# Optimization experiments

Measured on AMD Instinct MI355X. Metric: run time of the kernel, lower is better.

## Reference

```python
import jax, jax.numpy as jnp
import numpy as np

B, C, L = 8, 512, 2048


def setup_inputs() -> dict:
    key = jax.random.key(0)
    ks = jax.random.split(key, 7)
    s = 1.0 / np.sqrt(C)
    return {
        "x": jax.random.normal(ks[0], (B, C, L), dtype=jnp.float32),
        "Wq": jax.random.normal(ks[1], (C, C), dtype=jnp.float32) * s,
        "bq": jax.random.normal(ks[2], (C,), dtype=jnp.float32) * s,
        "Wk": jax.random.normal(ks[3], (C, C), dtype=jnp.float32) * s,
        "bk": jax.random.normal(ks[4], (C,), dtype=jnp.float32) * s,
        "Wv": jax.random.normal(ks[5], (C, C), dtype=jnp.float32) * s,
        "bv": jax.random.normal(ks[6], (C,), dtype=jnp.float32) * s,
    }


def reference(x, Wq, bq, Wk, bk, Wv, bv):
    # Conv1d(kernel_size=1) == per-position linear: [C_out, C_in] @ x[b,:,l]
    q = jnp.einsum('oi,bil->bol', Wq, x) + bq[None, :, None]  # [B, C, L]
    k = jnp.einsum('oi,bil->bol', Wk, x) + bk[None, :, None]
    v = jnp.einsum('oi,bil->bol', Wv, x) + bv[None, :, None]
    scale = 1.0 / jnp.sqrt(jnp.asarray(x.shape[1], dtype=x.dtype))
    # scores[b, l, m] = sum_c q[b,c,l] * k[b,c,m] / sqrt(C)
    scores = jnp.einsum('bcl,bcm->blm', q, k) * scale  # [B, L, L]
    attn = jax.nn.softmax(scores, axis=-1)
    # out[b, c, l] = sum_m v[b,c,m] * attn[b,l,m]   (== bmm(V, attn^T))
    return jnp.einsum('bcm,blm->bcl', v, attn)  # [B, C, L]
```

## Files before the change

### kernel.cpp

```cpp
#include <hip/hip_runtime.h>
#include <hip/hip_bf16.h>
#include <math.h>

#define B 8
#define C 512
#define L 2048

using bf16x8 = __bf16 __attribute__((ext_vector_type(8)));
using f32x4  = float __attribute__((ext_vector_type(4)));

#define MFMA(a, b, c) __builtin_amdgcn_mfma_f32_16x16x32_bf16((a), (b), (c), 0, 0, 0)
#define SC2 0.06375872f
#define SH2 -17.312340f

__device__ __forceinline__ unsigned short f2bf(float f) {
    unsigned int u; __builtin_memcpy(&u, &f, 4);
    u += 0x7FFF + ((u >> 16) & 1);
    return (unsigned short)(u >> 16);
}
__device__ __forceinline__ void load_lds16(const unsigned short* g, unsigned short* l) {
    __builtin_amdgcn_global_load_lds(
        (const __attribute__((address_space(1))) unsigned int*)g,
        (__attribute__((address_space(3))) unsigned int*)l, 16, 0, 0);
}

template<int MODE, int KDIM>
__device__ __forceinline__ void gemm_core(
    const unsigned short* __restrict__ A,
    const unsigned short* __restrict__ Bm,
    unsigned short* As, unsigned short* Bs,
    void* __restrict__ OutV, int ldo,
    float* __restrict__ ep)
{
    const int t = threadIdx.x;
    const int wave = t >> 6, lane = t & 63;
    const int ll = t & 15, quad = (t >> 4) & 3;
    const int lr = lane >> 2, chunk = lane & 3;
    const int wm = (wave & 1) * 64, wn = (wave >> 1) * 64;

    const unsigned short* gA0 = A  + (size_t)(wave * 32 + lr) * KDIM + chunk * 8;
    const unsigned short* gB0 = Bm + (size_t)(wave * 32 + lr) * KDIM + chunk * 8;
    unsigned short* lA0 = As + (wave * 32) * 32;
    unsigned short* lB0 = Bs + (wave * 32) * 32;
    const int P1 = 128 * 32;

    f32x4 acc[4][4];
#pragma unroll
    for (int i = 0; i < 4; ++i)
#pragma unroll
        for (int j = 0; j < 4; ++j) acc[i][j] = (f32x4){0.f, 0.f, 0.f, 0.f};

#pragma unroll 1
    for (int k0 = 0; k0 < KDIM; k0 += 64) {
        __syncthreads();
        load_lds16(gA0 + k0, lA0);
        load_lds16(gA0 + (size_t)16 * KDIM + k0, lA0 + 16 * 32);
        load_lds16(gA0 + k0 + 32, lA0 + P1);
        load_lds16(gA0 + (size_t)16 * KDIM + k0 + 32, lA0 + P1 + 16 * 32);
        load_lds16(gB0 + k0, lB0);
        load_lds16(gB0 + (size_t)16 * KDIM + k0, lB0 + 16 * 32);
        load_lds16(gB0 + k0 + 32, lB0 + P1);
        load_lds16(gB0 + (size_t)16 * KDIM + k0 + 32, lB0 + P1 + 16 * 32);
        __syncthreads();

#pragma unroll
        for (int p = 0; p < 2; ++p) {
            bf16x8 af[4], bf[4];
#pragma unroll
            for (int mi = 0; mi < 4; ++mi)
                af[mi] = *(const bf16x8*)&As[p * P1 + (wm + mi * 16 + ll) * 32 + quad * 8];
#pragma unroll
            for (int ni = 0; ni < 4; ++ni)
                bf[ni] = *(const bf16x8*)&Bs[p * P1 + (wn + ni * 16 + ll) * 32 + quad * 8];
#pragma unroll
            for (int mi = 0; mi < 4; ++mi)
#pragma unroll
                for (int ni = 0; ni < 4; ++ni)
                    acc[mi][ni] = MFMA(af[mi], bf[ni], acc[mi][ni]);
        }
    }

#pragma unroll
    for (int mi = 0; mi < 4; ++mi)
#pragma unroll
        for (int ni = 0; ni < 4; ++ni) {
            const int col = wn + ni * 16 + ll;
            float epc = 0.f;
            if (MODE == 0) epc = ep[col];
            if (MODE == 3) epc = 1.0f / ep[col];
#pragma unroll
            for (int r = 0; r < 4; ++r) {
                const int row = wm + mi * 16 + quad * 4 + r;
                float v = acc[mi][ni][r];
                if (MODE == 0)      v += epc;
                else if (MODE == 1) v += ep[row];
                else                v *= epc;
                if (MODE == 3)
                    ((float*)OutV)[(size_t)row * ldo + col] = v;
                else
                    ((unsigned short*)OutV)[(size_t)row * ldo + col] = f2bf(v);
            }
        }
}

__global__ __launch_bounds__(256) void prep(
    const float* __restrict__ x, const float* __restrict__ Wq,
    const float* __restrict__ Wk, const float* __restrict__ Wv,
    unsigned short* __restrict__ xt, unsigned short* __restrict__ o,
    float* __restrict__ rsum)
{
    __shared__ float tile[64][69];
    const int t = threadIdx.x;
    const int flat = blockIdx.x + 32 * (blockIdx.y + 8 * blockIdx.z);

    if (flat < 768) {
        if (flat < 16) {
            float4 z = make_float4(0.f, 0.f, 0.f, 0.f);
            *(float4*)(rsum + (flat * 256 + t) * 4) = z;
        }
        const int i = (flat * 256 + t) * 4;
        const int which = i >> 18;
        const int off = i & 0x3FFFF;
        const float* src = (which == 0) ? Wq : (which == 1) ? Wk : Wv;
        float4 v = *(const float4*)(src + off);
        union { unsigned short h[4]; uint2 u; } pk;
        pk.h[0] = f2bf(v.x); pk.h[1] = f2bf(v.y); pk.h[2] = f2bf(v.z); pk.h[3] = f2bf(v.w);
        *(uint2*)(o + i) = pk.u;
    }

    const int b = blockIdx.z, l0 = blockIdx.x * 64, c0 = blockIdx.y * 64;
    const int lx = t & 15, cy = t >> 4;
    const float* xb = x + (size_t)b * C * L;
#pragma unroll
    for (int p = 0; p < 4; ++p) {
        float4 v = *(const float4*)(xb + (size_t)(c0 + p * 16 + cy) * L + l0 + lx * 4);
        tile[p * 16 + cy][lx * 4 + 0] = v.x;
        tile[p * 16 + cy][lx * 4 + 1] = v.y;
        tile[p * 16 + cy][lx * 4 + 2] = v.z;
        tile[p * 16 + cy][lx * 4 + 3] = v.w;
    }
    __syncthreads();
    const int ocl = t & 15, ot = t >> 4;
    unsigned short* xtb = xt + (size_t)b * L * C;
#pragma unroll
    for (int p = 0; p < 4; ++p) {
        int ol = p * 16 + ot;
        union { unsigned short h[4]; uint2 u; } pk;
#pragma unroll
        for (int i = 0; i < 4; ++i) pk.h[i] = f2bf(tile[ocl * 4 + i][ol]);
        *(uint2*)(xtb + (size_t)(l0 + ol) * C + c0 + ocl * 4) = pk.u;
    }
}

__global__ __launch_bounds__(256) void qkv_gemm(
    const unsigned short* __restrict__ xt, const unsigned short* __restrict__ Wb,
    const float* __restrict__ bq, const float* __restrict__ bk,
    const float* __restrict__ bv,
    unsigned short* __restrict__ Qt, unsigned short* __restrict__ Kt,
    unsigned short* __restrict__ Vv)
{
    __shared__ unsigned short As[2 * 128 * 32], Bs[2 * 128 * 32];
    const int id = blockIdx.x;
    const int b = id & 7, r = id >> 3;
    const int which = r >> 6, tt = r & 63;
    const unsigned short* xtb = xt + (size_t)b * L * C;
    if (which < 2) {
        const int m0 = (tt & 15) * 128, n0 = (tt >> 4) * 128;
        const unsigned short* A  = xtb + (size_t)m0 * C;
        const unsigned short* Bm = Wb + (size_t)which * C * C + (size_t)n0 * C;
        unsigned short* Out = (which ? Kt : Qt) + (size_t)b * L * C
                              + (size_t)m0 * C + n0;
        gemm_core<0, C>(A, Bm, As, Bs, Out, C,
                        const_cast<float*>((which ? bk : bq) + n0));
    } else {
        const int m0 = (tt & 3) * 128, n0 = (tt >> 2) * 128;
        const unsigned short* A  = Wb + (size_t)2 * C * C + (size_t)m0 * C;
        const unsigned short* Bm = xtb + (size_t)n0 * C;
        unsigned short* Out = Vv + (size_t)b * C * L + (size_t)m0 * L + n0;
        gemm_core<1, C>(A, Bm, As, Bs, Out, L, const_cast<float*>(bv + m0));
    }
}

__global__ __launch_bounds__(512, 4) void sc_exp3(
    const unsigned short* __restrict__ Qt, const unsigned short* __restrict__ Kt,
    unsigned short* __restrict__ P, float* __restrict__ rsum,
    int hoff, int qrows, int mshift)
{
    __shared__ unsigned short As[256 * 64];
    __shared__ unsigned short Bs[128 * 64];
    constexpr int KD = C;

    const int id = blockIdx.x;
    const int b = id & 7, rr = id >> 3;
    const int m0 = (rr & ((1 << mshift) - 1)) * 256, n0 = (rr >> mshift) * 128;
    const unsigned short* A  = Qt + (size_t)b * L * C + (size_t)(hoff + m0) * C;
    const unsigned short* Bm = Kt + (size_t)b * L * C + (size_t)n0 * C;
    unsigned short* Out = P + (size_t)b * qrows * L + (size_t)m0 * L + n0;
    float* ep = rsum + (size_t)b * L + hoff + m0;

    const int t = threadIdx.x;
    const int wave = t >> 6, lane = t & 63;
    const int ll = t & 15, quad = (t >> 4) & 3;
    const int wm = (wave & 3) * 64, wn = (wave >> 2) * 64;

    const int r0 = t >> 3;
    const int swz = ((t & 7) ^ (r0 & 7)) * 8;
    const unsigned short* gA = A  + (size_t)r0 * KD + swz;
    const unsigned short* gB = Bm + (size_t)r0 * KD + swz;
    unsigned short* lA = As + wave * 512;
    unsigned short* lB = Bs + wave * 512;
    const int sw8 = ll & 7;

    f32x4 acc[4][4];
#pragma unroll
    for (int i = 0; i < 4; ++i)
#pragma unroll
        for (int j = 0; j < 4; ++j) acc[i][j] = (f32x4){0.f, 0.f, 0.f, 0.f};

#pragma unroll 1
    for (int k0 = 0; k0 < KD; k0 += 64) {
        __syncthreads();
        load_lds16(gA + k0,                     lA);
        load_lds16(gA + (size_t)64  * KD + k0,  lA + 64 * 64);
        load_lds16(gA + (size_t)128 * KD + k0,  lA + 128 * 64);
        load_lds16(gA + (size_t)192 * KD + k0,  lA + 192 * 64);
        load_lds16(gB + k0,                     lB);
        load_lds16(gB + (size_t)64  * KD + k0,  lB + 64 * 64);
        __syncthreads();

#pragma unroll
        for (int p = 0; p < 2; ++p) {
            bf16x8 af[4], bf[4];
#pragma unroll
            for (int mi = 0; mi < 4; ++mi)
                af[mi] = *(const bf16x8*)&As[(wm + mi * 16 + ll) * 64
                                             + ((p * 4 + quad) ^ sw8) * 8];
#pragma unroll
            for (int ni = 0; ni < 4; ++ni)
                bf[ni] = *(const bf16x8*)&Bs[(wn + ni * 16 + ll) * 64
                                             + ((p * 4 + quad) ^ sw8) * 8];
#pragma unroll
            for (int mi = 0; mi < 4; ++mi)
#pragma unroll
                for (int ni = 0; ni < 4; ++ni)
                    acc[mi][ni] = MFMA(af[mi], bf[ni], acc[mi][ni]);
        }
    }

    __syncthreads();
    unsigned* scratch = (unsigned*)As + wave * 1024;

    float rpart[4][4];
#pragma unroll
    for (int mi = 0; mi < 4; ++mi)
#pragma unroll
        for (int r = 0; r < 4; ++r) rpart[mi][r] = 0.f;

#pragma unroll
    for (int h = 0; h < 2; ++h) {
#pragma unroll
        for (int mi2 = 0; mi2 < 2; ++mi2) {
            const int mi = h * 2 + mi2;
#pragma unroll
            for (int ni = 0; ni < 4; ++ni)
#pragma unroll
                for (int r = 0; r < 4; ++r) {
                    float v = exp2f(fmaf(acc[mi][ni][r], SC2, SH2));
                    rpart[mi][r] += v;
                    unsigned bfv = f2bf(v);
                    unsigned pvv = (unsigned)__shfl_xor((int)bfv, 1, 64);
                    unsigned packed = (ll & 1) ? ((pvv & 0xFFFFu) | (bfv << 16))
                                               : ((bfv & 0xFFFFu) | (pvv << 16));
                    if (!(ll & 1))
                        scratch[(mi2 * 16 + quad * 4 + r) * 32 + ni * 8 + (ll >> 1)]
                            = packed;
                }
        }
#pragma unroll
        for (int i = 0; i < 4; ++i) {
            const int rl = i * 8 + (lane >> 3);
            uint4 d = *(const uint4*)(scratch + rl * 32 + (lane & 7) * 4);
            const int row = wm + h * 32 + rl;
            const int col = wn + (lane & 7) * 8;
            *(uint4*)&Out[(size_t)row * L + col] = d;
        }
    }

#pragma unroll
    for (int mi = 0; mi < 4; ++mi)
#pragma unroll
        for (int r = 0; r < 4; ++r) {
            float s = rpart[mi][r];
            s += __shfl_xor(s, 1, 64);
            s += __shfl_xor(s, 2, 64);
            s += __shfl_xor(s, 4, 64);
            s += __shfl_xor(s, 8, 64);
            if (ll == 0) atomicAdd(ep + wm + mi * 16 + quad * 4 + r, s);
        }
}

__global__ __launch_bounds__(256) void pv_gemm(
    const unsigned short* __restrict__ Vv, const unsigned short* __restrict__ P,
    const float* __restrict__ rsum, float* __restrict__ out,
    int hoff, int qrows)
{
    __shared__ unsigned short As[2 * 128 * 32], Bs[2 * 128 * 32];
    const int id = blockIdx.x;
    const int b = id & 7, r = id >> 3;
    const int m0 = (r & 3) * 128, n0 = (r >> 2) * 128;
    const unsigned short* A  = Vv + (size_t)b * C * L + (size_t)m0 * L;
    const unsigned short* Bm = P + (size_t)b * qrows * L + (size_t)n0 * L;
    float* Out = out + (size_t)b * C * L + (size_t)m0 * L + hoff + n0;
    float* ep = const_cast<float*>(rsum) + (size_t)b * L + hoff + n0;
    gemm_core<3, L>(A, Bm, As, Bs, Out, L, ep);
}

extern "C" void kernel_launch(void* const* d_in, const int* in_sizes, int n_in,
                              void* d_out, int out_size, void* d_ws, size_t ws_size,
                              hipStream_t stream) {
    const float* x  = (const float*)d_in[0];
    const float* Wq = (const float*)d_in[1];
    const float* bq = (const float*)d_in[2];
    const float* Wk = (const float*)d_in[3];
    const float* bk = (const float*)d_in[4];
    const float* Wv = (const float*)d_in[5];
    const float* bv = (const float*)d_in[6];
    float* out = (float*)d_out;

    const size_t BCL = (size_t)B * C * L;
    const bool fullP = ws_size >= 119078912ull;

    unsigned short* Qt = (unsigned short*)d_ws;
    unsigned short* Kt = Qt + BCL;
    unsigned short* Vv = Kt + BCL;
    unsigned short *Wb, *xt, *P;
    float* rsum;
    if (fullP) {
        Wb   = Vv + BCL;
        rsum = (float*)(Wb + (size_t)3 * C * C);
        xt   = (unsigned short*)(rsum + (size_t)B * L);
        P    = xt;
    } else {
        xt   = Vv + BCL;
        P    = xt;
        Wb   = P + (size_t)B * 1024 * L;
        rsum = (float*)(Wb + (size_t)3 * C * C);
    }

    prep<<<dim3(L / 64, C / 64, B), 256, 0, stream>>>(x, Wq, Wk, Wv, xt, Wb, rsum);
    qkv_gemm<<<dim3(1536), 256, 0, stream>>>(xt, Wb, bq, bk, bv, Qt, Kt, Vv);

    if (fullP) {
        sc_exp3<<<dim3(1024), 512, 0, stream>>>(Qt, Kt, P, rsum, 0, L, 3);
        pv_gemm<<<dim3(512), 256, 0, stream>>>(Vv, P, rsum, out, 0, L);
    } else {
        for (int h = 0; h < 2; ++h) {
            sc_exp3<<<dim3(512), 512, 0, stream>>>(Qt, Kt, P, rsum, h * 1024, 1024, 2);
            pv_gemm<<<dim3(256), 256, 0, stream>>>(Vv, P, rsum, out, h * 1024, 1024);
        }
    }
}
```

Baseline: 233.0 us.

## Add larger-tile PV GEMM kernel and write scores directly without LDS staging

Replaces the PV GEMM on the full-P path with a new 512-thread kernel. It uses 128x256 output tiles, a 64-deep K step and swizzled direct-to-LDS loads, and folds the 1/rowsum normalisation into its epilogue. The score/exp kernel also drops its LDS scratch repacking and the barrier before it, writing each bf16 probability straight to global memory. The larger tiles aim for more reuse per block. The direct scalar 2-byte stores remove a sync and LDS traffic but lose store coalescing and 16-byte vector writes. The new PV kernel has no double buffering and launches only 256 blocks, so it may leave compute units underused.

```diff
diff --git a/kernel.cpp b/kernel.cpp
--- a/kernel.cpp
+++ b/kernel.cpp
@@ -199,7 +199,7 @@
     float* ep = rsum + (size_t)b * L + hoff + m0;
 
     const int t = threadIdx.x;
-    const int wave = t >> 6, lane = t & 63;
+    const int wave = t >> 6;
     const int ll = t & 15, quad = (t >> 4) & 3;
     const int wm = (wave & 3) * 64, wn = (wave >> 2) * 64;
 
@@ -247,9 +247,6 @@
         }
     }
 
-    __syncthreads();
-    unsigned* scratch = (unsigned*)As + wave * 1024;
-
     float rpart[4][4];
 #pragma unroll
     for (int mi = 0; mi < 4; ++mi)
@@ -257,35 +254,18 @@
         for (int r = 0; r < 4; ++r) rpart[mi][r] = 0.f;
 
 #pragma unroll
-    for (int h = 0; h < 2; ++h) {
-#pragma unroll
-        for (int mi2 = 0; mi2 < 2; ++mi2) {
-            const int mi = h * 2 + mi2;
-#pragma unroll
-            for (int ni = 0; ni < 4; ++ni)
-#pragma unroll
-                for (int r = 0; r < 4; ++r) {
-                    float v = exp2f(fmaf(acc[mi][ni][r], SC2, SH2));
-                    rpart[mi][r] += v;
-                    unsigned bfv = f2bf(v);
-                    unsigned pvv = (unsigned)__shfl_xor((int)bfv, 1, 64);
-                    unsigned packed = (ll & 1) ? ((pvv & 0xFFFFu) | (bfv << 16))
-                                               : ((bfv & 0xFFFFu) | (pvv << 16));
-                    if (!(ll & 1))
-                        scratch[(mi2 * 16 + quad * 4 + r) * 32 + ni * 8 + (ll >> 1)]
-                            = packed;
-                }
-        }
-#pragma unroll
-        for (int i = 0; i < 4; ++i) {
-            const int rl = i * 8 + (lane >> 3);
-            uint4 d = *(const uint4*)(scratch + rl * 32 + (lane & 7) * 4);
-            const int row = wm + h * 32 + rl;
-            const int col = wn + (lane & 7) * 8;
-            *(uint4*)&Out[(size_t)row * L + col] = d;
-        }
-    }
-
+    for (int mi = 0; mi < 4; ++mi)
+#pragma unroll
+        for (int ni = 0; ni < 4; ++ni) {
+            const int col = wn + ni * 16 + ll;
+#pragma unroll
+            for (int r = 0; r < 4; ++r) {
+                const int row = wm + mi * 16 + quad * 4 + r;
+                float v = exp2f(fmaf(acc[mi][ni][r], SC2, SH2));
+                rpart[mi][r] += v;
+                Out[(size_t)row * L + col] = f2bf(v);
+            }
+        }
 #pragma unroll
     for (int mi = 0; mi < 4; ++mi)
 #pragma unroll
@@ -296,6 +276,84 @@
             s += __shfl_xor(s, 4, 64);
             s += __shfl_xor(s, 8, 64);
             if (ll == 0) atomicAdd(ep + wm + mi * 16 + quad * 4 + r, s);
+        }
+}
+
+__global__ __launch_bounds__(512, 4) void pv_gemm2(
+    const unsigned short* __restrict__ Vv, const unsigned short* __restrict__ P,
+    const float* __restrict__ rsum, float* __restrict__ out)
+{
+    __shared__ unsigned short As[128 * 64];
+    __shared__ unsigned short Bs[256 * 64];
+
+    const int id = blockIdx.x;
+    const int b = id & 7, rr = id >> 3;
+    const int m0 = (rr & 3) * 128, n0 = (rr >> 2) * 256;
+    const unsigned short* A  = Vv + (size_t)b * C * L + (size_t)m0 * L;
+    const unsigned short* Bm = P  + (size_t)b * L * L + (size_t)n0 * L;
+    float* Out = out + (size_t)b * C * L + (size_t)m0 * L + n0;
+    const float* ep = rsum + (size_t)b * L + n0;
+
+    const int t = threadIdx.x;
+    const int wave = t >> 6;
+    const int ll = t & 15, quad = (t >> 4) & 3;
+    const int wm = (wave & 1) * 64, wn = (wave >> 1) * 64;
+
+    const int r0 = t >> 3;
+    const int swz = ((t & 7) ^ (r0 & 7)) * 8;
+    const unsigned short* gA = A  + (size_t)r0 * L + swz;
+    const unsigned short* gB = Bm + (size_t)r0 * L + swz;
+    unsigned short* lA = As + wave * 512;
+    unsigned short* lB = Bs + wave * 512;
+    const int sw8 = ll & 7;
+
+    f32x4 acc[4][4];
+#pragma unroll
+    for (int i = 0; i < 4; ++i)
+#pragma unroll
+        for (int j = 0; j < 4; ++j) acc[i][j] = (f32x4){0.f, 0.f, 0.f, 0.f};
+
+#pragma unroll 1
+    for (int k0 = 0; k0 < L; k0 += 64) {
+        __syncthreads();
+        load_lds16(gA + k0,                    lA);
+        load_lds16(gA + (size_t)64  * L + k0,  lA + 64 * 64);
+        load_lds16(gB + k0,                    lB);
+        load_lds16(gB + (size_t)64  * L + k0,  lB + 64 * 64);
+        load_lds16(gB + (size_t)128 * L + k0,  lB + 128 * 64);
+        load_lds16(gB + (size_t)192 * L + k0,  lB + 192 * 64);
+        __syncthreads();
+
+#pragma unroll
+        for (int p = 0; p < 2; ++p) {
+            bf16x8 af[4], bf[4];
+#pragma unroll
+            for (int mi = 0; mi < 4; ++mi)
+                af[mi] = *(const bf16x8*)&As[(wm + mi * 16 + ll) * 64
+                                             + ((p * 4 + quad) ^ sw8) * 8];
+#pragma unroll
+            for (int ni = 0; ni < 4; ++ni)
+                bf[ni] = *(const bf16x8*)&Bs[(wn + ni * 16 + ll) * 64
+                                             + ((p * 4 + quad) ^ sw8) * 8];
+#pragma unroll
+            for (int mi = 0; mi < 4; ++mi)
+#pragma unroll
+                for (int ni = 0; ni < 4; ++ni)
+                    acc[mi][ni] = MFMA(af[mi], bf[ni], acc[mi][ni]);
+        }
+    }
+
+#pragma unroll
+    for (int mi = 0; mi < 4; ++mi)
+#pragma unroll
+        for (int ni = 0; ni < 4; ++ni) {
+            const int col = wn + ni * 16 + ll;
+            const float inv = 1.0f / ep[col];
+#pragma unroll
+            for (int r = 0; r < 4; ++r) {
+                const int row = wm + mi * 16 + quad * 4 + r;
+                Out[(size_t)row * L + col] = acc[mi][ni][r] * inv;
+            }
         }
 }
 
@@ -352,7 +410,7 @@
 
     if (fullP) {
         sc_exp3<<<dim3(1024), 512, 0, stream>>>(Qt, Kt, P, rsum, 0, L, 3);
-        pv_gemm<<<dim3(512), 256, 0, stream>>>(Vv, P, rsum, out, 0, L);
+        pv_gemm2<<<dim3(256), 512, 0, stream>>>(Vv, P, rsum, out);
     } else {
         for (int h = 0; h < 2; ++h) {
             sc_exp3<<<dim3(512), 512, 0, stream>>>(Qt, Kt, P, rsum, h * 1024, 1024, 2);
```

Result: faster. 221.4 us (-5.0%).
